# Performance work log

Measured on AMD Instinct MI355X. Metric: run time of the kernel, lower is better.

Reference implementation:

```python
import jax, jax.numpy as jnp
import numpy as np

D_EMBED = 1024
N_HEADS = 16
BATCH = 2
SEQ = 2048


def setup_inputs() -> dict:
    key = jax.random.key(0)
    k1, k2, k3 = jax.random.split(key, 3)
    scale = 0.02
    x = jax.random.normal(k1, (BATCH, SEQ, D_EMBED), dtype=jnp.float32)
    w_qkv = jax.random.normal(k2, (D_EMBED, 3 * D_EMBED), dtype=jnp.float32) * scale
    b_qkv = jnp.zeros((3 * D_EMBED,), dtype=jnp.float32)
    w_o = jax.random.normal(k3, (D_EMBED, D_EMBED), dtype=jnp.float32) * scale
    b_o = jnp.zeros((D_EMBED,), dtype=jnp.float32)
    return {"x": x, "w_qkv": w_qkv, "b_qkv": b_qkv, "w_o": w_o, "b_o": b_o}


def reference(x, w_qkv, b_qkv, w_o, b_o):
    bs, sl, ed = x.shape
    nh = N_HEADS
    hd = ed // nh
    # fused QKV projection, split into q, k, v
    qkv = x @ w_qkv + b_qkv                      # [bs, sl, 3*ed]
    q, k, v = jnp.split(qkv, 3, axis=2)
    # [bs, sl, (nh hd)] -> [bs, nh, sl, hd]
    def heads(t):
        return t.reshape(bs, sl, nh, hd).transpose(0, 2, 1, 3)
    q, k, v = heads(q), heads(k), heads(v)
    # scaled dot-product attention with causal mask (full SxS scores, as in the original)
    scores = jnp.einsum('bhqd,bhkd->bhqk', q, k) / jnp.sqrt(jnp.float32(hd))
    causal = jnp.tril(jnp.ones((sl, sl), dtype=bool))
    scores = jnp.where(causal[None, None, :, :], scores, jnp.float32(-jnp.inf))
    attn = jax.nn.softmax(scores, axis=-1)       # dropout p=0 -> identity
    out = jnp.einsum('bhqk,bhkd->bhqd', attn, v) # [bs, nh, sl, hd]
    out = out.transpose(0, 2, 1, 3).reshape(bs, sl, ed)
    return out @ w_o + b_o
```

## Files before the change

### kernel.cpp

```cpp
#include <hip/hip_runtime.h>
#include <hip/hip_bf16.h>

typedef __hip_bfloat16 bf16;
typedef unsigned short u16;
typedef __attribute__((ext_vector_type(8))) short short8;
typedef __attribute__((ext_vector_type(4))) float floatx4;

#define D_EMBED 1024
#define N_HEADS 16
#define HEAD_DIM 64
#define BATCH 2
#define SEQ 2048
#define ROWS (BATCH * SEQ)
#define QKV_COLS (3 * D_EMBED)
#define QSCALE 0.1803368801f

__device__ __forceinline__ void g2l16(const void* g, void* l) {
    __builtin_amdgcn_global_load_lds(
        (const __attribute__((address_space(1))) unsigned int*)g,
        (__attribute__((address_space(3))) unsigned int*)l,
        16, 0, 0);
}

__device__ __forceinline__ u16 f2b_bits(float f) {
    bf16 h = __float2bfloat16(f);
    u16 u;
    __builtin_memcpy(&u, &h, 2);
    return u;
}

__device__ __forceinline__ unsigned pack2(float a, float b) {
    return (unsigned)f2b_bits(a) | ((unsigned)f2b_bits(b) << 16);
}

__device__ __forceinline__ float fexp2(float x) {
#if __has_builtin(__builtin_amdgcn_exp2f)
    return __builtin_amdgcn_exp2f(x);
#else
    return exp2f(x);
#endif
}

__device__ __forceinline__ unsigned permpack(float a, float b) {
#if __has_builtin(__builtin_amdgcn_perm)
    return __builtin_amdgcn_perm(__float_as_uint(b), __float_as_uint(a), 0x07060302u);
#else
    return (__float_as_uint(a) >> 16) | (__float_as_uint(b) & 0xFFFF0000u);
#endif
}

__global__ __launch_bounds__(256)
void prep(const float* __restrict__ x, const float* __restrict__ w_qkv,
          const float* __restrict__ w_o, bf16* __restrict__ xb,
          bf16* __restrict__ wqkvT, bf16* __restrict__ woT)
{
    __shared__ u16 T[64][72];
    const int tid = threadIdx.x;
    const int bid = blockIdx.x;

    if (bid < 4096) {
        const int i = bid * 256 + tid;
        const float4 v = reinterpret_cast<const float4*>(x)[i];
        ushort4 o;
        o.x = f2b_bits(v.x); o.y = f2b_bits(v.y);
        o.z = f2b_bits(v.z); o.w = f2b_bits(v.w);
        reinterpret_cast<ushort4*>(xb)[i] = o;
        return;
    }
    const float* in; u16* out; int R, C, bx, by;
    if (bid < 4864) {
        const int t = bid - 4096;
        in = w_qkv; out = reinterpret_cast<u16*>(wqkvT); R = 1024; C = 3072;
        bx = t % 48; by = t / 48;
    } else {
        const int t = bid - 4864;
        in = w_o; out = reinterpret_cast<u16*>(woT); R = 1024; C = 1024;
        bx = t % 16; by = t / 16;
    }
    const int r0 = by * 64, c0 = bx * 64;
#pragma unroll
    for (int it = 0; it < 4; ++it) {
        const int r = (tid >> 4) + it * 16;
        const int c4 = (tid & 15) * 4;
        const float4 v = *reinterpret_cast<const float4*>(in + (size_t)(r0 + r) * C + c0 + c4);
        T[c4 + 0][r] = f2b_bits(v.x);
        T[c4 + 1][r] = f2b_bits(v.y);
        T[c4 + 2][r] = f2b_bits(v.z);
        T[c4 + 3][r] = f2b_bits(v.w);
    }
    __syncthreads();
#pragma unroll
    for (int it = 0; it < 4; ++it) {
        const int rr = (tid >> 4) + it * 16;
        const int cc4 = (tid & 15) * 4;
        ushort4 o = *reinterpret_cast<const ushort4*>(&T[rr][cc4]);
        *reinterpret_cast<ushort4*>(out + (size_t)(c0 + rr) * R + r0 + cc4) = o;
    }
}

__global__ __launch_bounds__(256)
void gemm_qkv(const bf16* __restrict__ A, const bf16* __restrict__ Bt,
              const float* __restrict__ bias,
              bf16* __restrict__ qb, bf16* __restrict__ kb, bf16* __restrict__ vtb)
{
    __shared__ __align__(16) char smem[32768];
    char* BUF0 = smem;
    char* BUF1 = smem + 16384;

    const int tid = threadIdx.x;
    const int lane = tid & 63, w = tid >> 6;
    const int quad = lane >> 4, l15 = lane & 15;
    const int mw = (w >> 1) * 64, nw = (w & 1) * 64;
    const int blockM = blockIdx.y * 128, blockN = blockIdx.x * 128;

    const int row0 = tid >> 2, ch = tid & 3;
    const int off0 = (tid & ~63) * 16;
    const bf16* Asrc0 = A + (size_t)(blockM + row0) * 1024 + ch * 8;
    const bf16* Asrc1 = Asrc0 + (size_t)64 * 1024;
    const bf16* Bsrc0 = Bt + (size_t)(blockN + row0) * 1024 + ch * 8;
    const bf16* Bsrc1 = Bsrc0 + (size_t)64 * 1024;

    auto stage = [&](int k0, char* buf) {
        g2l16(Asrc0 + k0, buf + off0);
        g2l16(Asrc1 + k0, buf + off0 + 4096);
        g2l16(Bsrc0 + k0, buf + 8192 + off0);
        g2l16(Bsrc1 + k0, buf + 8192 + off0 + 4096);
    };

    floatx4 acc[4][4];
#pragma unroll
    for (int i = 0; i < 4; ++i)
#pragma unroll
        for (int j = 0; j < 4; ++j) acc[i][j] = (floatx4){0.f, 0.f, 0.f, 0.f};

    auto compute = [&](char* buf) {
        short8 af[4], bfr[4];
#pragma unroll
        for (int mi = 0; mi < 4; ++mi)
            af[mi] = *reinterpret_cast<const short8*>(
                buf + (mw + mi * 16 + l15) * 64 + quad * 16);
#pragma unroll
        for (int ni = 0; ni < 4; ++ni)
            bfr[ni] = *reinterpret_cast<const short8*>(
                buf + 8192 + (nw + ni * 16 + l15) * 64 + quad * 16);
#pragma unroll
        for (int mi = 0; mi < 4; ++mi)
#pragma unroll
            for (int ni = 0; ni < 4; ++ni)
                acc[mi][ni] = __builtin_amdgcn_mfma_f32_16x16x32_bf16(
                    af[mi], bfr[ni], acc[mi][ni], 0, 0, 0);
    };

    stage(0, BUF0);
    __syncthreads();
#pragma unroll 1
    for (int k0 = 0; k0 < 1024; k0 += 64) {
        if (k0 + 32 < 1024) stage(k0 + 32, BUF1);
        compute(BUF0);
        __syncthreads();
        if (k0 + 64 < 1024) stage(k0 + 64, BUF0);
        compute(BUF1);
        __syncthreads();
    }

    u16* W = reinterpret_cast<u16*>(smem + w * 2304);
    const bool isq = (blockN < 1024);
    const bool isv = (blockN >= 2048);

    float bvn[4];
#pragma unroll
    for (int ni = 0; ni < 4; ++ni) bvn[ni] = bias[blockN + nw + ni * 16 + l15];

    if (!isv) {
        bf16* dstbuf = isq ? qb : kb;
        const int coloff = blockN - (isq ? 0 : 1024);
#pragma unroll
        for (int mi = 0; mi < 4; ++mi) {
#pragma unroll
            for (int ni = 0; ni < 4; ++ni) {
#pragma unroll
                for (int r = 0; r < 4; ++r) {
                    float val = acc[mi][ni][r] + bvn[ni];
                    if (isq) val *= QSCALE;
                    W[(quad * 4 + r) * 72 + ni * 16 + l15] = f2b_bits(val);
                }
            }
#pragma unroll
            for (int half = 0; half < 2; ++half) {
                const int idx = half * 64 + lane;
                const int rowL = idx >> 3, chh = idx & 7;
                short8 v = *reinterpret_cast<const short8*>(W + rowL * 72 + chh * 8);
                const int grow = blockM + mw + mi * 16 + rowL;
                const int gcol = coloff + nw + chh * 8;
                *reinterpret_cast<short8*>(
                    reinterpret_cast<u16*>(dstbuf) + (size_t)grow * 1024 + gcol) = v;
            }
        }
    } else {
        const int col0 = blockN - 2048 + nw;
        const int h = col0 >> 6;
        const int bh = (blockM >> 11) * 16 + h;
        const int sb = (blockM & 2047) + mw;
        u16* vdst = reinterpret_cast<u16*>(vtb) + (size_t)bh * 64 * SEQ;
#pragma unroll
        for (int mi = 0; mi < 4; ++mi) {
#pragma unroll
            for (int ni = 0; ni < 4; ++ni) {
#pragma unroll
                for (int r = 0; r < 4; ++r)
                    W[(quad * 4 + r) * 72 + ni * 16 + l15] =
                        f2b_bits(acc[mi][ni][r] + bvn[ni]);
            }
#pragma unroll
            for (int mc = 0; mc < 2; ++mc) {
                u16 tmp[8];
#pragma unroll
                for (int e = 0; e < 8; ++e) tmp[e] = W[(mc * 8 + e) * 72 + lane];
                const int s = sb + mi * 16 + mc * 8;
                *reinterpret_cast<short8*>(vdst + (size_t)lane * SEQ + s) =
                    *reinterpret_cast<const short8*>(tmp);
            }
        }
    }
}

__global__ __launch_bounds__(256)
void gemm_out(const bf16* __restrict__ A, const bf16* __restrict__ Bt,
              const float* __restrict__ bias, float* __restrict__ outf)
{
    __shared__ __align__(16) char smem[24576];
    char* BUF0 = smem;
    char* BUF1 = smem + 12288;

    const int tid = threadIdx.x;
    const int lane = tid & 63, w = tid >> 6;
    const int quad = lane >> 4, l15 = lane & 15;
    const int mw = (w >> 1) * 64, nw = (w & 1) * 32;
    const int blockM = blockIdx.y * 128, blockN = blockIdx.x * 64;

    const int row0 = tid >> 2, ch = tid & 3;
    const int off0 = (tid & ~63) * 16;
    const bf16* Asrc0 = A + (size_t)(blockM + row0) * 1024 + ch * 8;
    const bf16* Asrc1 = Asrc0 + (size_t)64 * 1024;
    const bf16* Bsrc0 = Bt + (size_t)(blockN + row0) * 1024 + ch * 8;

    auto stage = [&](int k0, char* buf) {
        g2l16(Asrc0 + k0, buf + off0);
        g2l16(Asrc1 + k0, buf + off0 + 4096);
        g2l16(Bsrc0 + k0, buf + 8192 + off0);
    };

    floatx4 acc[4][2];
#pragma unroll
    for (int i = 0; i < 4; ++i)
#pragma unroll
        for (int j = 0; j < 2; ++j) acc[i][j] = (floatx4){0.f, 0.f, 0.f, 0.f};

    auto compute = [&](char* buf) {
        short8 af[4], bfr[2];
#pragma unroll
        for (int mi = 0; mi < 4; ++mi)
            af[mi] = *reinterpret_cast<const short8*>(
                buf + (mw + mi * 16 + l15) * 64 + quad * 16);
#pragma unroll
        for (int ni = 0; ni < 2; ++ni)
            bfr[ni] = *reinterpret_cast<const short8*>(
                buf + 8192 + (nw + ni * 16 + l15) * 64 + quad * 16);
#pragma unroll
        for (int mi = 0; mi < 4; ++mi)
#pragma unroll
            for (int ni = 0; ni < 2; ++ni)
                acc[mi][ni] = __builtin_amdgcn_mfma_f32_16x16x32_bf16(
                    af[mi], bfr[ni], acc[mi][ni], 0, 0, 0);
    };

    stage(0, BUF0);
    __syncthreads();
#pragma unroll 1
    for (int k0 = 0; k0 < 1024; k0 += 64) {
        if (k0 + 32 < 1024) stage(k0 + 32, BUF1);
        compute(BUF0);
        __syncthreads();
        if (k0 + 64 < 1024) stage(k0 + 64, BUF0);
        compute(BUF1);
        __syncthreads();
    }

    float bvn[2];
#pragma unroll
    for (int ni = 0; ni < 2; ++ni) bvn[ni] = bias[blockN + nw + ni * 16 + l15];

#pragma unroll
    for (int mi = 0; mi < 4; ++mi)
#pragma unroll
        for (int r = 0; r < 4; ++r) {
            const int row = blockM + mw + mi * 16 + quad * 4 + r;
#pragma unroll
            for (int ni = 0; ni < 2; ++ni) {
                const int col = blockN + nw + ni * 16 + l15;
                outf[(size_t)row * 1024 + col] = acc[mi][ni][r] + bvn[ni];
            }
        }
}

__global__ __launch_bounds__(256)
void attn_mfma(const bf16* __restrict__ qb, const bf16* __restrict__ kb,
               const bf16* __restrict__ vtb, bf16* __restrict__ ob)
{
    __shared__ __align__(16) char smem[49152];
    char* KV0 = smem;
    char* KV1 = smem + 16384;
    const int tid = threadIdx.x;
    const int lane = tid & 63, w = tid >> 6;
    const int quad = lane >> 4, l15 = lane & 15;
    char* PsB = smem + 32768 + w * 2048;
    char* PsS = smem + 40960 + w * 2048;

    const int l = blockIdx.x;
    const int bh = l & 31;
    const int slot = l >> 5;
    const int pi = (slot < 8) ? slot : 23 - slot;
    const int b = bh >> 4, h = bh & 15;

    const int qtS = pi, qtB = 31 - pi;
    const int q0S = qtS * 64, q0B = qtB * 64;
    const int KT = qtB + 1;
    const int qrowS = q0S + w * 16 + l15;
    const int qrowB = q0B + w * 16 + l15;

    const size_t kvrow = (size_t)b * SEQ;
    const size_t vbase = (size_t)bh * 64 * SEQ;

    const short8 ones = {0x3F80, 0x3F80, 0x3F80, 0x3F80,
                         0x3F80, 0x3F80, 0x3F80, 0x3F80};

    const int row0 = tid >> 3;
    const int lch = (tid & 7) ^ (row0 & 7);
    const int loff0 = (tid & ~63) * 16;
    const int loff1 = loff0 + 4096;
    const bf16* ksrc0 = kb + (kvrow + row0) * D_EMBED + h * 64 + lch * 8;
    const bf16* ksrc1 = ksrc0 + (size_t)32 * D_EMBED;
    const bf16* vsrc0 = vtb + vbase + (size_t)row0 * SEQ + lch * 8;
    const bf16* vsrc1 = vsrc0 + (size_t)32 * SEQ;

    {
        const bf16* qsrcS = qb + (kvrow + q0S + row0) * D_EMBED + h * 64 + lch * 8;
        const bf16* qsrcB = qb + (kvrow + q0B + row0) * D_EMBED + h * 64 + lch * 8;
        g2l16(qsrcS, KV1 + loff0);
        g2l16(qsrcS + (size_t)32 * D_EMBED, KV1 + loff1);
        g2l16(qsrcB, KV1 + 8192 + loff0);
        g2l16(qsrcB + (size_t)32 * D_EMBED, KV1 + 8192 + loff1);
        g2l16(ksrc0, KV0 + loff0);
        g2l16(ksrc1, KV0 + loff1);
        g2l16(vsrc0, KV0 + 8192 + loff0);
        g2l16(vsrc1, KV0 + 8192 + loff1);
    }
    __syncthreads();

    const int qoff = (w * 16 + l15) * 128;
    const int x0 = (quad ^ (l15 & 7)) * 16;
    const int x1 = ((quad + 4) ^ (l15 & 7)) * 16;
    const short8 qS0 = *reinterpret_cast<const short8*>(KV1 + qoff + x0);
    const short8 qS1 = *reinterpret_cast<const short8*>(KV1 + qoff + x1);
    const short8 qB0 = *reinterpret_cast<const short8*>(KV1 + 8192 + qoff + x0);
    const short8 qB1 = *reinterpret_cast<const short8*>(KV1 + 8192 + qoff + x1);
    __syncthreads();

    floatx4 OaccS[4], OaccB[4], LaccS, LaccB;
#pragma unroll
    for (int i = 0; i < 4; ++i) {
        OaccS[i] = (floatx4){0.f, 0.f, 0.f, 0.f};
        OaccB[i] = (floatx4){0.f, 0.f, 0.f, 0.f};
    }
    LaccS = (floatx4){0.f, 0.f, 0.f, 0.f};
    LaccB = (floatx4){0.f, 0.f, 0.f, 0.f};

    auto prefetch = [&](int nkt, char* dst) {
        const size_t ko = (size_t)nkt * 64;
        g2l16(ksrc0 + ko * D_EMBED, dst + loff0);
        g2l16(ksrc1 + ko * D_EMBED, dst + loff1);
        g2l16(vsrc0 + ko, dst + 8192 + loff0);
        g2l16(vsrc1 + ko, dst + 8192 + loff1);
    };

    auto compute = [&](int kt, char* Ks, char* Vs) {
        const int k0 = kt * 64;
        const bool doS = (kt <= qtS);
        short8 kf[2][4], vf[2][4];
#pragma unroll
        for (int ms = 0; ms < 4; ++ms) {
            const int roff = (ms * 16 + l15) * 128;
            kf[0][ms] = *reinterpret_cast<const short8*>(Ks + roff + x0);
            kf[1][ms] = *reinterpret_cast<const short8*>(Ks + roff + x1);
        }
#pragma unroll
        for (int ks = 0; ks < 2; ++ks)
#pragma unroll
            for (int ds = 0; ds < 4; ++ds)
                vf[ks][ds] = *reinterpret_cast<const short8*>(
                    Vs + (ds * 16 + l15) * 128 + (((quad + ks * 4) ^ (l15 & 7)) * 16));

        floatx4 SB[4], SS[4];
#pragma unroll
        for (int ms = 0; ms < 4; ++ms) {
            floatx4 t = (floatx4){0.f, 0.f, 0.f, 0.f};
            t = __builtin_amdgcn_mfma_f32_16x16x32_bf16(kf[0][ms], qB0, t, 0, 0, 0);
            SB[ms] = __builtin_amdgcn_mfma_f32_16x16x32_bf16(kf[1][ms], qB1, t, 0, 0, 0);
        }
        if (doS) {
#pragma unroll
            for (int ms = 0; ms < 4; ++ms) {
                floatx4 t = (floatx4){0.f, 0.f, 0.f, 0.f};
                t = __builtin_amdgcn_mfma_f32_16x16x32_bf16(kf[0][ms], qS0, t, 0, 0, 0);
                SS[ms] = __builtin_amdgcn_mfma_f32_16x16x32_bf16(kf[1][ms], qS1, t, 0, 0, 0);
            }
        }

        const bool diagB = (kt == KT - 1);
#pragma unroll
        for (int ms = 0; ms < 4; ++ms) {
            float p[4];
#pragma unroll
            for (int r = 0; r < 4; ++r) {
                float s = SB[ms][r];
                if (diagB && (k0 + ms * 16 + quad * 4 + r) > qrowB) s = -1e30f;
                p[r] = fexp2(s);
            }
            const int k = ms * 16 + quad * 4;
            uint2 pw;
            pw.x = permpack(p[0], p[1]);
            pw.y = permpack(p[2], p[3]);
            *reinterpret_cast<uint2*>(PsB + (k >> 3) * 256 + l15 * 16 + (k & 7) * 2) = pw;
        }
        if (doS) {
            const bool diagS = (kt == qtS);
#pragma unroll
            for (int ms = 0; ms < 4; ++ms) {
                float p[4];
#pragma unroll
                for (int r = 0; r < 4; ++r) {
                    float s = SS[ms][r];
                    if (diagS && (k0 + ms * 16 + quad * 4 + r) > qrowS) s = -1e30f;
                    p[r] = fexp2(s);
                }
                const int k = ms * 16 + quad * 4;
                uint2 pw;
                pw.x = permpack(p[0], p[1]);
                pw.y = permpack(p[2], p[3]);
                *reinterpret_cast<uint2*>(PsS + (k >> 3) * 256 + l15 * 16 + (k & 7) * 2) = pw;
            }
        }

#pragma unroll
        for (int ks = 0; ks < 2; ++ks) {
            const short8 pfB = *reinterpret_cast<const short8*>(
                PsB + (ks * 4 + quad) * 256 + l15 * 16);
            LaccB = __builtin_amdgcn_mfma_f32_16x16x32_bf16(ones, pfB, LaccB, 0, 0, 0);
#pragma unroll
            for (int ds = 0; ds < 4; ++ds)
                OaccB[ds] = __builtin_amdgcn_mfma_f32_16x16x32_bf16(
                    vf[ks][ds], pfB, OaccB[ds], 0, 0, 0);
            if (doS) {
                const short8 pfS = *reinterpret_cast<const short8*>(
                    PsS + (ks * 4 + quad) * 256 + l15 * 16);
                LaccS = __builtin_amdgcn_mfma_f32_16x16x32_bf16(ones, pfS, LaccS, 0, 0, 0);
#pragma unroll
                for (int ds = 0; ds < 4; ++ds)
                    OaccS[ds] = __builtin_amdgcn_mfma_f32_16x16x32_bf16(
                        vf[ks][ds], pfS, OaccS[ds], 0, 0, 0);
            }
        }
    };

#pragma unroll 1
    for (int kt = 0; kt < KT; kt += 2) {
        if (kt + 1 < KT) prefetch(kt + 1, KV1);
        compute(kt, KV0, KV0 + 8192);
        __syncthreads();
        if (kt + 1 >= KT) break;
        if (kt + 2 < KT) prefetch(kt + 2, KV0);
        compute(kt + 1, KV1, KV1 + 8192);
        __syncthreads();
    }

#pragma unroll
    for (int which = 0; which < 2; ++which) {
        const floatx4* Oacc = which ? OaccB : OaccS;
        const float invl = 1.f / (which ? LaccB[0] : LaccS[0]);
        const int q0 = which ? q0B : q0S;
#pragma unroll
        for (int ds = 0; ds < 4; ++ds) {
            const int d = ds * 16 + quad * 4;
            uint2 ow;
            ow.x = pack2(Oacc[ds][0] * invl, Oacc[ds][1] * invl);
            ow.y = pack2(Oacc[ds][2] * invl, Oacc[ds][3] * invl);
            *reinterpret_cast<uint2*>(
                PsB + (d >> 3) * 256 + l15 * 16 + (d & 7) * 2) = ow;
        }
#pragma unroll
        for (int it = 0; it < 2; ++it) {
            const int idx = it * 64 + lane;
            const int chh = idx >> 4, q = idx & 15;
            short8 ov = *reinterpret_cast<const short8*>(PsB + chh * 256 + q * 16);
            *reinterpret_cast<short8*>(
                ob + (kvrow + q0 + w * 16 + q) * D_EMBED + h * 64 + chh * 8) = ov;
        }
    }
}

extern "C" void kernel_launch(void* const* d_in, const int* in_sizes, int n_in,
                              void* d_out, int out_size, void* d_ws, size_t ws_size,
                              hipStream_t stream)
{
    const float* x     = (const float*)d_in[0];
    const float* w_qkv = (const float*)d_in[1];
    const float* b_qkv = (const float*)d_in[2];
    const float* w_o   = (const float*)d_in[3];
    const float* b_o   = (const float*)d_in[4];
    float* out = (float*)d_out;

    bf16* xb     = (bf16*)d_ws;
    bf16* wqkvT  = xb + (size_t)4096 * 1024;
    bf16* woT    = wqkvT + (size_t)3072 * 1024;
    bf16* qbuf   = woT + (size_t)1024 * 1024;
    bf16* kbuf   = qbuf + (size_t)4096 * 1024;
    bf16* vtb    = kbuf + (size_t)4096 * 1024;
    bf16* attnb  = vtb + (size_t)4096 * 1024;

    dim3 blk(256);

    prep<<<dim3(5120), blk, 0, stream>>>(x, w_qkv, w_o, xb, wqkvT, woT);

    gemm_qkv<<<dim3(24, 32), blk, 0, stream>>>(xb, wqkvT, b_qkv, qbuf, kbuf, vtb);

    attn_mfma<<<dim3(512), blk, 0, stream>>>(qbuf, kbuf, vtb, attnb);

    gemm_out<<<dim3(16, 32), blk, 0, stream>>>(attnb, woT, b_o, out);
}
```

Baseline: 175.0 us.

## Software-pipeline attention PV MFMAs one tile behind QK and softmax

```diff
diff --git a/kernel.cpp b/kernel.cpp
--- a/kernel.cpp
+++ b/kernel.cpp
@@ -307,14 +307,17 @@
 void attn_mfma(const bf16* __restrict__ qb, const bf16* __restrict__ kb,
                const bf16* __restrict__ vtb, bf16* __restrict__ ob)
 {
-    __shared__ __align__(16) char smem[49152];
+    __shared__ __align__(16) char smem[65536];
     char* KV0 = smem;
     char* KV1 = smem + 16384;
     const int tid = threadIdx.x;
     const int lane = tid & 63, w = tid >> 6;
     const int quad = lane >> 4, l15 = lane & 15;
-    char* PsB = smem + 32768 + w * 2048;
-    char* PsS = smem + 40960 + w * 2048;
+    char* PsW  = smem + 32768 + w * 8192;
+    char* PsB0 = PsW;
+    char* PsS0 = PsW + 2048;
+    char* PsB1 = PsW + 4096;
+    char* PsS1 = PsW + 6144;
 
     const int l = blockIdx.x;
     const int bh = l & 31;
@@ -375,6 +378,8 @@
     LaccS = (floatx4){0.f, 0.f, 0.f, 0.f};
     LaccB = (floatx4){0.f, 0.f, 0.f, 0.f};
 
+    short8 vfA[2][4], vfB[2][4];
+
     auto prefetch = [&](int nkt, char* dst) {
         const size_t ko = (size_t)nkt * 64;
         g2l16(ksrc0 + ko * D_EMBED, dst + loff0);
@@ -383,24 +388,43 @@
         g2l16(vsrc1 + ko, dst + 8192 + loff1);
     };
 
-    auto compute = [&](int kt, char* Ks, char* Vs) {
+    auto compute = [&](int kt, char* Ks, char* Vs,
+                       char* PsWb, char* PsWs, char* PsRb, char* PsRs,
+                       short8 (&vfC)[2][4], short8 (&vfP)[2][4]) {
         const int k0 = kt * 64;
-        const bool doS = (kt <= qtS);
-        short8 kf[2][4], vf[2][4];
+        const bool doS   = (kt <= qtS);
+        const bool prevB = (kt > 0);
+        const bool prevS = prevB && (kt - 1 <= qtS);
+
+        short8 kf[2][4];
 #pragma unroll
         for (int ms = 0; ms < 4; ++ms) {
             const int roff = (ms * 16 + l15) * 128;
             kf[0][ms] = *reinterpret_cast<const short8*>(Ks + roff + x0);
             kf[1][ms] = *reinterpret_cast<const short8*>(Ks + roff + x1);
         }
+        short8 pfPB[2], pfPS[2];
+        if (prevB) {
+#pragma unroll
+            for (int ks = 0; ks < 2; ++ks)
+                pfPB[ks] = *reinterpret_cast<const short8*>(
+                    PsRb + (ks * 4 + quad) * 256 + l15 * 16);
+        }
+        if (prevS) {
+#pragma unroll
+            for (int ks = 0; ks < 2; ++ks)
+                pfPS[ks] = *reinterpret_cast<const short8*>(
+                    PsRs + (ks * 4 + quad) * 256 + l15 * 16);
+        }
 #pragma unroll
         for (int ks = 0; ks < 2; ++ks)
 #pragma unroll
             for (int ds = 0; ds < 4; ++ds)
-                vf[ks][ds] = *reinterpret_cast<const short8*>(
+                vfC[ks][ds] = *reinterpret_cast<const short8*>(
                     Vs + (ds * 16 + l15) * 128 + (((quad + ks * 4) ^ (l15 & 7)) * 16));
 
         floatx4 SB[4], SS[4];
+        __builtin_amdgcn_s_setprio(1);
 #pragma unroll
         for (int ms = 0; ms < 4; ++ms) {
             floatx4 t = (floatx4){0.f, 0.f, 0.f, 0.f};
@@ -415,6 +439,27 @@
                 SS[ms] = __builtin_amdgcn_mfma_f32_16x16x32_bf16(kf[1][ms], qS1, t, 0, 0, 0);
             }
         }
+        if (prevB) {
+#pragma unroll
+            for (int ks = 0; ks < 2; ++ks) {
+                LaccB = __builtin_amdgcn_mfma_f32_16x16x32_bf16(ones, pfPB[ks], LaccB, 0, 0, 0);
+#pragma unroll
+                for (int ds = 0; ds < 4; ++ds)
+                    OaccB[ds] = __builtin_amdgcn_mfma_f32_16x16x32_bf16(
+                        vfP[ks][ds], pfPB[ks], OaccB[ds], 0, 0, 0);
+            }
+        }
+        if (prevS) {
+#pragma unroll
+            for (int ks = 0; ks < 2; ++ks) {
+                LaccS = __builtin_amdgcn_mfma_f32_16x16x32_bf16(ones, pfPS[ks], LaccS, 0, 0, 0);
+#pragma unroll
+                for (int ds = 0; ds < 4; ++ds)
+                    OaccS[ds] = __builtin_amdgcn_mfma_f32_16x16x32_bf16(
+                        vfP[ks][ds], pfPS[ks], OaccS[ds], 0, 0, 0);
+            }
+        }
+        __builtin_amdgcn_s_setprio(0);
 
         const bool diagB = (kt == KT - 1);
 #pragma unroll
@@ -430,7 +475,7 @@
             uint2 pw;
             pw.x = permpack(p[0], p[1]);
             pw.y = permpack(p[2], p[3]);
-            *reinterpret_cast<uint2*>(PsB + (k >> 3) * 256 + l15 * 16 + (k & 7) * 2) = pw;
+            *reinterpret_cast<uint2*>(PsWb + (k >> 3) * 256 + l15 * 16 + (k & 7) * 2) = pw;
         }
         if (doS) {
             const bool diagS = (kt == qtS);
@@ -447,27 +492,7 @@
                 uint2 pw;
                 pw.x = permpack(p[0], p[1]);
                 pw.y = permpack(p[2], p[3]);
-                *reinterpret_cast<uint2*>(PsS + (k >> 3) * 256 + l15 * 16 + (k & 7) * 2) = pw;
-            }
-        }
-
-#pragma unroll
-        for (int ks = 0; ks < 2; ++ks) {
-            const short8 pfB = *reinterpret_cast<const short8*>(
-                PsB + (ks * 4 + quad) * 256 + l15 * 16);
-            LaccB = __builtin_amdgcn_mfma_f32_16x16x32_bf16(ones, pfB, LaccB, 0, 0, 0);
-#pragma unroll
-            for (int ds = 0; ds < 4; ++ds)
-                OaccB[ds] = __builtin_amdgcn_mfma_f32_16x16x32_bf16(
-                    vf[ks][ds], pfB, OaccB[ds], 0, 0, 0);
-            if (doS) {
-                const short8 pfS = *reinterpret_cast<const short8*>(
-                    PsS + (ks * 4 + quad) * 256 + l15 * 16);
-                LaccS = __builtin_amdgcn_mfma_f32_16x16x32_bf16(ones, pfS, LaccS, 0, 0, 0);
-#pragma unroll
-                for (int ds = 0; ds < 4; ++ds)
-                    OaccS[ds] = __builtin_amdgcn_mfma_f32_16x16x32_bf16(
-                        vf[ks][ds], pfS, OaccS[ds], 0, 0, 0);
+                *reinterpret_cast<uint2*>(PsWs + (k >> 3) * 256 + l15 * 16 + (k & 7) * 2) = pw;
             }
         }
     };
@@ -475,12 +500,29 @@
 #pragma unroll 1
     for (int kt = 0; kt < KT; kt += 2) {
         if (kt + 1 < KT) prefetch(kt + 1, KV1);
-        compute(kt, KV0, KV0 + 8192);
+        compute(kt, KV0, KV0 + 8192, PsB0, PsS0, PsB1, PsS1, vfA, vfB);
         __syncthreads();
         if (kt + 1 >= KT) break;
         if (kt + 2 < KT) prefetch(kt + 2, KV0);
-        compute(kt + 1, KV1, KV1 + 8192);
+        compute(kt + 1, KV1, KV1 + 8192, PsB1, PsS1, PsB0, PsS0, vfB, vfA);
         __syncthreads();
+    }
+
+    {
+        auto finishB = [&](char* R, short8 (&vfP)[2][4]) {
+#pragma unroll
+            for (int ks = 0; ks < 2; ++ks) {
+                const short8 pf = *reinterpret_cast<const short8*>(
+                    R + (ks * 4 + quad) * 256 + l15 * 16);
+                LaccB = __builtin_amdgcn_mfma_f32_16x16x32_bf16(ones, pf, LaccB, 0, 0, 0);
+#pragma unroll
+                for (int ds = 0; ds < 4; ++ds)
+                    OaccB[ds] = __builtin_amdgcn_mfma_f32_16x16x32_bf16(
+                        vfP[ks][ds], pf, OaccB[ds], 0, 0, 0);
+            }
+        };
+        if (((KT - 1) & 1) == 0) finishB(PsB0, vfA);
+        else                     finishB(PsB1, vfB);
     }
 
 #pragma unroll
@@ -495,13 +537,13 @@
             ow.x = pack2(Oacc[ds][0] * invl, Oacc[ds][1] * invl);
             ow.y = pack2(Oacc[ds][2] * invl, Oacc[ds][3] * invl);
             *reinterpret_cast<uint2*>(
-                PsB + (d >> 3) * 256 + l15 * 16 + (d & 7) * 2) = ow;
+                PsB0 + (d >> 3) * 256 + l15 * 16 + (d & 7) * 2) = ow;
         }
 #pragma unroll
         for (int it = 0; it < 2; ++it) {
             const int idx = it * 64 + lane;
             const int chh = idx >> 4, q = idx & 15;
-            short8 ov = *reinterpret_cast<const short8*>(PsB + chh * 256 + q * 16);
+            short8 ov = *reinterpret_cast<const short8*>(PsB0 + chh * 256 + q * 16);
             *reinterpret_cast<short8*>(
                 ob + (kvrow + q0 + w * 16 + q) * D_EMBED + h * 64 + chh * 8) = ov;
         }
```

Result: slower. 202.5 us (+15.7%).

## Double K/V tile pairs per sync and raise MFMA wave priority

Applied to the files above, without the earlier changes.

```diff
diff --git a/kernel.cpp b/kernel.cpp
--- a/kernel.cpp
+++ b/kernel.cpp
@@ -307,14 +307,16 @@
 void attn_mfma(const bf16* __restrict__ qb, const bf16* __restrict__ kb,
                const bf16* __restrict__ vtb, bf16* __restrict__ ob)
 {
-    __shared__ __align__(16) char smem[49152];
-    char* KV0 = smem;
-    char* KV1 = smem + 16384;
+    __shared__ __align__(16) char smem[81920];
+    char* A0 = smem;
+    char* A1 = smem + 16384;
+    char* B0 = smem + 32768;
+    char* B1 = smem + 49152;
     const int tid = threadIdx.x;
     const int lane = tid & 63, w = tid >> 6;
     const int quad = lane >> 4, l15 = lane & 15;
-    char* PsB = smem + 32768 + w * 2048;
-    char* PsS = smem + 40960 + w * 2048;
+    char* PsB = smem + 65536 + w * 2048;
+    char* PsS = smem + 73728 + w * 2048;
 
     const int l = blockIdx.x;
     const int bh = l & 31;
@@ -343,38 +345,6 @@
     const bf16* vsrc0 = vtb + vbase + (size_t)row0 * SEQ + lch * 8;
     const bf16* vsrc1 = vsrc0 + (size_t)32 * SEQ;
 
-    {
-        const bf16* qsrcS = qb + (kvrow + q0S + row0) * D_EMBED + h * 64 + lch * 8;
-        const bf16* qsrcB = qb + (kvrow + q0B + row0) * D_EMBED + h * 64 + lch * 8;
-        g2l16(qsrcS, KV1 + loff0);
-        g2l16(qsrcS + (size_t)32 * D_EMBED, KV1 + loff1);
-        g2l16(qsrcB, KV1 + 8192 + loff0);
-        g2l16(qsrcB + (size_t)32 * D_EMBED, KV1 + 8192 + loff1);
-        g2l16(ksrc0, KV0 + loff0);
-        g2l16(ksrc1, KV0 + loff1);
-        g2l16(vsrc0, KV0 + 8192 + loff0);
-        g2l16(vsrc1, KV0 + 8192 + loff1);
-    }
-    __syncthreads();
-
-    const int qoff = (w * 16 + l15) * 128;
-    const int x0 = (quad ^ (l15 & 7)) * 16;
-    const int x1 = ((quad + 4) ^ (l15 & 7)) * 16;
-    const short8 qS0 = *reinterpret_cast<const short8*>(KV1 + qoff + x0);
-    const short8 qS1 = *reinterpret_cast<const short8*>(KV1 + qoff + x1);
-    const short8 qB0 = *reinterpret_cast<const short8*>(KV1 + 8192 + qoff + x0);
-    const short8 qB1 = *reinterpret_cast<const short8*>(KV1 + 8192 + qoff + x1);
-    __syncthreads();
-
-    floatx4 OaccS[4], OaccB[4], LaccS, LaccB;
-#pragma unroll
-    for (int i = 0; i < 4; ++i) {
-        OaccS[i] = (floatx4){0.f, 0.f, 0.f, 0.f};
-        OaccB[i] = (floatx4){0.f, 0.f, 0.f, 0.f};
-    }
-    LaccS = (floatx4){0.f, 0.f, 0.f, 0.f};
-    LaccB = (floatx4){0.f, 0.f, 0.f, 0.f};
-
     auto prefetch = [&](int nkt, char* dst) {
         const size_t ko = (size_t)nkt * 64;
         g2l16(ksrc0 + ko * D_EMBED, dst + loff0);
@@ -383,6 +353,36 @@
         g2l16(vsrc1 + ko, dst + 8192 + loff1);
     };
 
+    {
+        const bf16* qsrcS = qb + (kvrow + q0S + row0) * D_EMBED + h * 64 + lch * 8;
+        const bf16* qsrcB = qb + (kvrow + q0B + row0) * D_EMBED + h * 64 + lch * 8;
+        g2l16(qsrcS, B0 + loff0);
+        g2l16(qsrcS + (size_t)32 * D_EMBED, B0 + loff1);
+        g2l16(qsrcB, B0 + 8192 + loff0);
+        g2l16(qsrcB + (size_t)32 * D_EMBED, B0 + 8192 + loff1);
+        prefetch(0, A0);
+        prefetch(1, A1);
+    }
+    __syncthreads();
+
+    const int qoff = (w * 16 + l15) * 128;
+    const int x0 = (quad ^ (l15 & 7)) * 16;
+    const int x1 = ((quad + 4) ^ (l15 & 7)) * 16;
+    const short8 qS0 = *reinterpret_cast<const short8*>(B0 + qoff + x0);
+    const short8 qS1 = *reinterpret_cast<const short8*>(B0 + qoff + x1);
+    const short8 qB0 = *reinterpret_cast<const short8*>(B0 + 8192 + qoff + x0);
+    const short8 qB1 = *reinterpret_cast<const short8*>(B0 + 8192 + qoff + x1);
+    __syncthreads();
+
+    floatx4 OaccS[4], OaccB[4], LaccS, LaccB;
+#pragma unroll
+    for (int i = 0; i < 4; ++i) {
+        OaccS[i] = (floatx4){0.f, 0.f, 0.f, 0.f};
+        OaccB[i] = (floatx4){0.f, 0.f, 0.f, 0.f};
+    }
+    LaccS = (floatx4){0.f, 0.f, 0.f, 0.f};
+    LaccB = (floatx4){0.f, 0.f, 0.f, 0.f};
+
     auto compute = [&](int kt, char* Ks, char* Vs) {
         const int k0 = kt * 64;
         const bool doS = (kt <= qtS);
@@ -401,6 +401,7 @@
                     Vs + (ds * 16 + l15) * 128 + (((quad + ks * 4) ^ (l15 & 7)) * 16));
 
         floatx4 SB[4], SS[4];
+        __builtin_amdgcn_s_setprio(1);
 #pragma unroll
         for (int ms = 0; ms < 4; ++ms) {
             floatx4 t = (floatx4){0.f, 0.f, 0.f, 0.f};
@@ -415,6 +416,7 @@
                 SS[ms] = __builtin_amdgcn_mfma_f32_16x16x32_bf16(kf[1][ms], qS1, t, 0, 0, 0);
             }
         }
+        __builtin_amdgcn_s_setprio(0);
 
         const bool diagB = (kt == KT - 1);
 #pragma unroll
@@ -451,6 +453,7 @@
             }
         }
 
+        __builtin_amdgcn_s_setprio(1);
 #pragma unroll
         for (int ks = 0; ks < 2; ++ks) {
             const short8 pfB = *reinterpret_cast<const short8*>(
@@ -470,16 +473,21 @@
                         vf[ks][ds], pfS, OaccS[ds], 0, 0, 0);
             }
         }
+        __builtin_amdgcn_s_setprio(0);
     };
 
 #pragma unroll 1
-    for (int kt = 0; kt < KT; kt += 2) {
-        if (kt + 1 < KT) prefetch(kt + 1, KV1);
-        compute(kt, KV0, KV0 + 8192);
+    for (int kt = 0; kt < KT; kt += 4) {
+        if (kt + 2 < KT) prefetch(kt + 2, B0);
+        if (kt + 3 < KT) prefetch(kt + 3, B1);
+        compute(kt, A0, A0 + 8192);
+        if (kt + 1 < KT) compute(kt + 1, A1, A1 + 8192);
         __syncthreads();
-        if (kt + 1 >= KT) break;
-        if (kt + 2 < KT) prefetch(kt + 2, KV0);
-        compute(kt + 1, KV1, KV1 + 8192);
+        if (kt + 2 >= KT) break;
+        if (kt + 4 < KT) prefetch(kt + 4, A0);
+        if (kt + 5 < KT) prefetch(kt + 5, A1);
+        compute(kt + 2, B0, B0 + 8192);
+        if (kt + 3 < KT) compute(kt + 3, B1, B1 + 8192);
         __syncthreads();
     }
 
```

Measured after the change: 172.9 us. No clear change (-1.2%).
